# Optimization experiments

Measured on AMD Instinct MI355X. Metric: run time of the kernel, lower is better.

Reference implementation:

```python
import jax, jax.numpy as jnp
import numpy as np

K_TOP = 2          # hardcoded k in MyAttentionFunction
S = 32             # hardcoded spatial size (interpolate to 32x32)
N = S * S          # 1024 patches (patch_size=1, stride=1 unfold)
NEG = jnp.float32(-1e30)  # stand-in for excluding columns from top-k


def setup_inputs() -> dict:
    key = jax.random.key(0)
    k1, k2, k3 = jax.random.split(key, 3)
    C = 4096
    generated = jax.random.normal(k1, (1, C, S, S), dtype=jnp.float32)
    known = jax.random.normal(k2, (1, C, S, S), dtype=jnp.float32)
    mask = jax.random.randint(k3, (1, 1, S, S), 0, 2).astype(jnp.float32)
    return {"generated": generated, "known": known, "mask": mask}


def _forward(generated, known, mask):
    C = generated.shape[1]
    # F.interpolate(mask, (32,32)) nearest, then flatten -> flag in {0,1}, shape (N,)
    flag = jax.image.resize(mask, (1, 1, S, S), method="nearest").reshape(N)
    # MyUnfold(x, 1, 1) == [1, N, C]; drop batch dim of 1.
    P = generated.reshape(C, N).T   # (N, C) patches of `generated`
    Kp = known.reshape(C, N).T      # (N, C) patches of `known`

    norm_p = jnp.sum(P * P, axis=-1)   # (N,)
    norm_k = jnp.sum(Kp * Kp, axis=-1)
    # Full cosine matrices; original restricts rows to flag==1 and columns to
    # flag==0 (cosine0) / flag==1 (cosine1) by extraction; we mask columns with
    # a very negative value so top-k returns the same values with GLOBAL indices
    # (which is exactly what the original reconstructs via nonzero()[indexes]).
    cos0 = (P @ Kp.T) / jnp.sqrt(norm_p[:, None] * norm_k[None, :])  # (N, N)
    cos1 = (P @ P.T) / jnp.sqrt(norm_p[:, None] * norm_p[None, :])
    cos0 = jnp.where(flag[None, :] == 0, cos0, NEG)
    cos1 = jnp.where(flag[None, :] == 1, cos1, NEG)

    w0, i0 = jax.lax.top_k(cos0, K_TOP)  # (N, k) values / global indices
    w1, i1 = jax.lax.top_k(cos1, K_TOP)

    m = flag                      # 1.0 on masked rows
    nm = jnp.sum(m)               # number of masked patches
    # weight means taken only over masked rows, then softmax (original uses
    # .item() + numpy softmax, i.e. detached constants).
    means = jnp.stack(
        [jnp.sum(w0[:, i] * m) / nm for i in range(K_TOP)]
        + [jnp.sum(w1[:, i] * m) / nm for i in range(K_TOP)]
    )
    weights = jax.lax.stop_gradient(jax.nn.softmax(means))  # (2k,)

    # The original builds dense 1024x1024 indicator matrices and bmm's them;
    # each indicator row for a masked patch is one-hot at its retrieved source,
    # so the bmm is just a gather into masked rows. The advanced-indexing quirk
    # ind[mask_idx, src_idx] (nonzero() pairs include a leading 0 column) also
    # unconditionally sets ind[0,0]=1; we reproduce that (set semantics: no
    # double count if row 0 already maps to column 0).
    rtn = jnp.zeros((N, C), dtype=generated.dtype)
    for i in range(2 * K_TOP):
        src = Kp if i < K_TOP else P
        cols = (i0 if i < K_TOP else i1)[:, i % K_TOP]  # (N,) global indices
        out_i = jnp.where(m[:, None] == 1, src[cols], 0.0)  # masked rows only
        dup = 1.0 - ((m[0] == 1) & (cols[0] == 0)).astype(src.dtype)
        out_i = out_i.at[0].add(src[0] * dup)  # spurious ind[0,0]=1 artifact
        rtn = rtn + weights[i] * out_i

    rtn = rtn.reshape(1, S, S, C).transpose(0, 3, 1, 2)  # (1, C, 32, 32)
    return jnp.concatenate([generated, known, rtn], axis=1)


def reference(generated, known, mask):
    return _forward(generated, known, mask)
```

## Files before the change

### kernel.cpp

```cpp
#include <hip/hip_runtime.h>
#include <hip/hip_bf16.h>
#include <math.h>

#define N_TOT 1024
#define C_DIM 4096
#define T_MARGIN 3e-4f

typedef __attribute__((ext_vector_type(8))) _Float16 half8;
typedef __attribute__((ext_vector_type(8))) unsigned short ushort8;
typedef __attribute__((ext_vector_type(4))) float floatx4;

__device__ inline unsigned short f2h(float v) {
    _Float16 h = (_Float16)v;
    return __builtin_bit_cast(unsigned short, h);
}
__device__ inline float h2f(unsigned short u) {
    return (float)__builtin_bit_cast(_Float16, u);
}

__global__ __launch_bounds__(256) void split_norms(const float* __restrict__ G,
                                                   const float* __restrict__ Kn,
                                                   unsigned short* __restrict__ Phi,
                                                   unsigned short* __restrict__ Plo,
                                                   unsigned short* __restrict__ Khi,
                                                   unsigned short* __restrict__ Klo,
                                                   float* __restrict__ normP,
                                                   float* __restrict__ normK) {
    const int z = blockIdx.z;
    const float* X = z ? Kn : G;
    unsigned short* Xhi = z ? Khi : Phi;
    unsigned short* Xlo = z ? Klo : Plo;
    float* normX = z ? normK : normP;

    __shared__ float tile[64 * 65];
    __shared__ float np[256];
    const int t  = threadIdx.x;
    const int c0 = blockIdx.x * 64;
    const int n0 = blockIdx.y * 64;

    float s2 = 0.0f;
    #pragma unroll
    for (int s = 0; s < 16; s++) {
        int c_loc = s * 4 + (t >> 6);
        int n_loc = t & 63;
        float v = X[(c0 + c_loc) * N_TOT + n0 + n_loc];
        tile[c_loc * 65 + n_loc] = v;
        s2 = fmaf(v, v, s2);
    }
    np[t] = s2;
    __syncthreads();

    if (t < 64) {
        float tot = np[t] + np[t + 64] + np[t + 128] + np[t + 192];
        atomicAdd(&normX[n0 + t], tot);
    }

    #pragma unroll
    for (int s = 0; s < 4; s++) {
        int n_loc = s * 16 + (t >> 4);
        int c4    = (t & 15) * 4;
        unsigned short h[4], l[4];
        #pragma unroll
        for (int e = 0; e < 4; e++) {
            float v = tile[(c4 + e) * 65 + n_loc];
            h[e] = f2h(v);
            l[e] = f2h(v - h2f(h[e]));
        }
        size_t base = (size_t)(n0 + n_loc) * C_DIM + c0 + c4;
        *(ushort4*)&Xhi[base] = make_ushort4(h[0], h[1], h[2], h[3]);
        *(ushort4*)&Xlo[base] = make_ushort4(l[0], l[1], l[2], l[3]);
    }
}

__global__ __launch_bounds__(256, 2) void gemm_coarse(const unsigned short* __restrict__ Phi,
                                                      const unsigned short* __restrict__ Bcat,
                                                      float* __restrict__ dotAll) {
    __shared__ unsigned short sA[128 * 64];
    __shared__ unsigned short sB[128 * 64];

    const int t    = threadIdx.x;
    const int wave = t >> 6, lane = t & 63;
    const int wm   = wave >> 1, wn = wave & 1;
    const int quad = lane >> 4, lrow = lane & 15;
    const int ib = blockIdx.x * 128, jb = blockIdx.y * 128;
    const int k_beg = blockIdx.z * 1024;

    const int srow = t >> 3;
    const int g    = (t & 7) ^ (srow & 7);

    const unsigned short* gA = Phi  + (size_t)(ib + srow) * C_DIM + g * 8;
    const unsigned short* gB = Bcat + (size_t)(jb + srow) * C_DIM + g * 8;
    const size_t rstep = (size_t)32 * C_DIM;

    floatx4 acc[4][4] = {};

    for (int k0 = k_beg; k0 < k_beg + 1024; k0 += 64) {
        #pragma unroll
        for (int q = 0; q < 4; q++) {
            int lds_off = q * 4096 + t * 16;
            __builtin_amdgcn_global_load_lds(
                (const __attribute__((address_space(1))) void*)(gA + q * rstep + k0),
                (__attribute__((address_space(3))) void*)((char*)sA + lds_off), 16, 0, 0);
            __builtin_amdgcn_global_load_lds(
                (const __attribute__((address_space(1))) void*)(gB + q * rstep + k0),
                (__attribute__((address_space(3))) void*)((char*)sB + lds_off), 16, 0, 0);
        }
        __syncthreads();

        #pragma unroll
        for (int kk = 0; kk < 2; kk++) {
            const int gk = kk * 4 + quad;
            half8 a[4], b[4];
            #pragma unroll
            for (int ti = 0; ti < 4; ti++) {
                int m = wm * 64 + ti * 16 + lrow;
                a[ti] = *(const half8*)&sA[m * 64 + ((gk ^ (m & 7)) << 3)];
            }
            #pragma unroll
            for (int tj = 0; tj < 4; tj++) {
                int n = wn * 64 + tj * 16 + lrow;
                b[tj] = *(const half8*)&sB[n * 64 + ((gk ^ (n & 7)) << 3)];
            }
            #pragma unroll
            for (int ti = 0; ti < 4; ti++)
                #pragma unroll
                for (int tj = 0; tj < 4; tj++)
                    acc[ti][tj] = __builtin_amdgcn_mfma_f32_16x16x32_f16(a[ti], b[tj], acc[ti][tj], 0, 0, 0);
        }
        __syncthreads();
    }

    #pragma unroll
    for (int tj = 0; tj < 4; tj++) {
        int j = jb + wn * 64 + tj * 16 + lrow;
        #pragma unroll
        for (int ti = 0; ti < 4; ti++) {
            #pragma unroll
            for (int reg = 0; reg < 4; reg++) {
                int i = ib + wm * 64 + ti * 16 + quad * 4 + reg;
                atomicAdd(&dotAll[(size_t)i * 2048 + j], acc[ti][tj][reg]);
            }
        }
    }
}

__global__ __launch_bounds__(256) void topk_refine(const float* __restrict__ dotAll,
                                                   const unsigned short* __restrict__ Phi,
                                                   const unsigned short* __restrict__ Plo,
                                                   const unsigned short* __restrict__ Khi,
                                                   const unsigned short* __restrict__ Klo,
                                                   const float* __restrict__ normP,
                                                   const float* __restrict__ normK,
                                                   const float* __restrict__ flag,
                                                   float* __restrict__ w01,
                                                   int* __restrict__ i01) {
    __shared__ float sAf[C_DIM];
    __shared__ float s_bv[4];
    __shared__ int   s_bj[4];
    __shared__ float s_rcv[8];

    const int row = blockIdx.x;
    const int z   = blockIdx.y;
    const int t   = threadIdx.x;
    const int wave = t >> 6, lane = t & 63;
    const float* D  = dotAll + (size_t)row * 2048 + z * 1024;
    const float* nB = z ? normP : normK;
    const float target = z ? 1.0f : 0.0f;
    const float nr = normP[row];

    float4 dv = *(const float4*)(D + 4 * t);
    float4 fv = *(const float4*)(flag + 4 * t);
    float4 nv = *(const float4*)(nB + 4 * t);
    float cv[4];
    cv[0] = (fv.x == target) ? dv.x * rsqrtf(nr * nv.x) : -INFINITY;
    cv[1] = (fv.y == target) ? dv.y * rsqrtf(nr * nv.y) : -INFINITY;
    cv[2] = (fv.z == target) ? dv.z * rsqrtf(nr * nv.z) : -INFINITY;
    cv[3] = (fv.w == target) ? dv.w * rsqrtf(nr * nv.w) : -INFINITY;

    int   cand[8];
    float cval[8];
    #pragma unroll
    for (int it = 0; it < 8; it++) {
        float bv = cv[0]; int bj = 4 * t;
        #pragma unroll
        for (int e = 1; e < 4; e++) {
            int j = 4 * t + e;
            if (cv[e] > bv || (cv[e] == bv && j < bj)) { bv = cv[e]; bj = j; }
        }
        #pragma unroll
        for (int off = 32; off > 0; off >>= 1) {
            float ov = __shfl_xor(bv, off);
            int   oj = __shfl_xor(bj, off);
            if (ov > bv || (ov == bv && oj < bj)) { bv = ov; bj = oj; }
        }
        if (lane == 0) { s_bv[wave] = bv; s_bj[wave] = bj; }
        __syncthreads();
        float wv = s_bv[0]; int wj = s_bj[0];
        #pragma unroll
        for (int w = 1; w < 4; w++) {
            if (s_bv[w] > wv || (s_bv[w] == wv && s_bj[w] < wj)) { wv = s_bv[w]; wj = s_bj[w]; }
        }
        cand[it] = wj; cval[it] = wv;
        #pragma unroll
        for (int e = 0; e < 4; e++)
            if (wj == 4 * t + e) cv[e] = -INFINITY;
        __syncthreads();
    }

    const bool trust = (cval[0] - cval[1] > T_MARGIN) && (cval[1] - cval[2] > T_MARGIN);
    if (trust) {
        if (t == 0) {
            int base = (z * N_TOT + row) * 2;
            w01[base]     = cval[0];
            w01[base + 1] = cval[1];
            i01[base]     = cand[0];
            i01[base + 1] = cand[1];
        }
        return;
    }

    const unsigned short* Ah = Phi + (size_t)row * C_DIM;
    const unsigned short* Al = Plo + (size_t)row * C_DIM;
    const unsigned short* Bh = z ? Phi : Khi;
    const unsigned short* Bl = z ? Plo : Klo;

    #pragma unroll
    for (int s = 0; s < 2; s++) {
        int c = t * 16 + s * 8;
        ushort8 hb = *(const ushort8*)&Ah[c];
        ushort8 lb = *(const ushort8*)&Al[c];
        #pragma unroll
        for (int e = 0; e < 8; e++) sAf[c + e] = h2f(hb[e]) + h2f(lb[e]);
    }
    __syncthreads();

    const int grp = t >> 5, l32 = t & 31;
    const unsigned short* bh_row = Bh + (size_t)cand[grp] * C_DIM;
    const unsigned short* bl_row = Bl + (size_t)cand[grp] * C_DIM;
    float acc = 0.0f;
    for (int it = 0; it < 16; it++) {
        int c = it * 256 + l32 * 8;
        ushort8 hb = *(const ushort8*)&bh_row[c];
        ushort8 lb = *(const ushort8*)&bl_row[c];
        #pragma unroll
        for (int e = 0; e < 8; e++)
            acc = fmaf(sAf[c + e], h2f(hb[e]) + h2f(lb[e]), acc);
    }
    #pragma unroll
    for (int off = 16; off > 0; off >>= 1) acc += __shfl_xor(acc, off);
    if (l32 == 0) s_rcv[grp] = acc;
    __syncthreads();

    if (t == 0) {
        float v1 = -INFINITY, v2 = -INFINITY;
        int   j1 = 0x7FFFFFFF, j2 = 0x7FFFFFFF;
        #pragma unroll
        for (int q = 0; q < 8; q++) {
            int j = cand[q];
            float cvx = s_rcv[q] * rsqrtf(nr * nB[j]);
            if (cvx > v1 || (cvx == v1 && j < j1)) {
                v2 = v1; j2 = j1; v1 = cvx; j1 = j;
            } else if (cvx > v2 || (cvx == v2 && j < j2)) {
                v2 = cvx; j2 = j;
            }
        }
        int base = (z * N_TOT + row) * 2;
        w01[base]     = v1;
        w01[base + 1] = v2;
        i01[base]     = j1;
        i01[base + 1] = j2;
    }
}

__global__ __launch_bounds__(256) void output_kernel(const float* __restrict__ G,
                                                     const float* __restrict__ Kn,
                                                     const float* __restrict__ flag,
                                                     const float* __restrict__ w01,
                                                     const int* __restrict__ i01,
                                                     float* __restrict__ out) {
    __shared__ float red[5][4];
    __shared__ float wts[4];
    const int c  = blockIdx.x;
    const int t  = threadIdx.x;
    const int n4 = t * 4;

    float4 fv = *(const float4*)&flag[n4];
    const float fa[4] = {fv.x, fv.y, fv.z, fv.w};

    float pm[5] = {};
    #pragma unroll
    for (int e = 0; e < 4; e++) {
        int n = n4 + e;
        float m = fa[e];
        pm[0] += m;
        pm[1] += m * w01[n * 2 + 0];
        pm[2] += m * w01[n * 2 + 1];
        pm[3] += m * w01[2 * N_TOT + n * 2 + 0];
        pm[4] += m * w01[2 * N_TOT + n * 2 + 1];
    }
    #pragma unroll
    for (int i = 0; i < 5; i++)
        #pragma unroll
        for (int off = 32; off > 0; off >>= 1)
            pm[i] += __shfl_xor(pm[i], off);
    const int wave = t >> 6, lane = t & 63;
    if (lane == 0) {
        #pragma unroll
        for (int i = 0; i < 5; i++) red[i][wave] = pm[i];
    }
    __syncthreads();
    if (t == 0) {
        float tot[5];
        #pragma unroll
        for (int i = 0; i < 5; i++)
            tot[i] = red[i][0] + red[i][1] + red[i][2] + red[i][3];
        float inv = 1.0f / tot[0];
        float mv[4] = {tot[1] * inv, tot[2] * inv, tot[3] * inv, tot[4] * inv};
        float mx = fmaxf(fmaxf(mv[0], mv[1]), fmaxf(mv[2], mv[3]));
        float e[4], s = 0.0f;
        #pragma unroll
        for (int q = 0; q < 4; q++) { e[q] = expf(mv[q] - mx); s += e[q]; }
        #pragma unroll
        for (int q = 0; q < 4; q++) wts[q] = e[q] / s;
    }
    __syncthreads();
    const float w0 = wts[0], w1 = wts[1], w2 = wts[2], w3 = wts[3];

    float4 gv = *(const float4*)&G[c * N_TOT + n4];
    float4 kv = *(const float4*)&Kn[c * N_TOT + n4];
    *(float4*)&out[c * N_TOT + n4] = gv;
    *(float4*)&out[C_DIM * N_TOT + c * N_TOT + n4] = kv;

    float val[4];
    #pragma unroll
    for (int e = 0; e < 4; e++) {
        int n = n4 + e;
        float v = 0.0f;
        if (fa[e] == 1.0f) {
            int c00 = i01[n * 2 + 0];
            int c01 = i01[n * 2 + 1];
            int c10 = i01[2 * N_TOT + n * 2 + 0];
            int c11 = i01[2 * N_TOT + n * 2 + 1];
            v = w0 * Kn[c * N_TOT + c00] + w1 * Kn[c * N_TOT + c01]
              + w2 * G[c * N_TOT + c10]  + w3 * G[c * N_TOT + c11];
        }
        if (n == 0) {
            bool m0 = (flag[0] == 1.0f);
            int c00 = i01[0], c01 = i01[1];
            int c10 = i01[2 * N_TOT], c11 = i01[2 * N_TOT + 1];
            float kn0 = Kn[c * N_TOT];
            float g0  = G[c * N_TOT];
            if (!(m0 && c00 == 0)) v += w0 * kn0;
            if (!(m0 && c01 == 0)) v += w1 * kn0;
            if (!(m0 && c10 == 0)) v += w2 * g0;
            if (!(m0 && c11 == 0)) v += w3 * g0;
        }
        val[e] = v;
    }
    *(float4*)&out[2 * C_DIM * N_TOT + c * N_TOT + n4] =
        make_float4(val[0], val[1], val[2], val[3]);
}

extern "C" void kernel_launch(void* const* d_in, const int* in_sizes, int n_in,
                              void* d_out, int out_size, void* d_ws, size_t ws_size,
                              hipStream_t stream) {
    const float* G    = (const float*)d_in[0];
    const float* Kn   = (const float*)d_in[1];
    const float* flag = (const float*)d_in[2];
    float* out = (float*)d_out;

    unsigned short* Khi = (unsigned short*)d_ws;
    unsigned short* Phi = Khi + (size_t)N_TOT * C_DIM;
    unsigned short* Klo = Phi + (size_t)N_TOT * C_DIM;
    unsigned short* Plo = Klo + (size_t)N_TOT * C_DIM;
    float* dotAll = (float*)(Plo + (size_t)N_TOT * C_DIM);
    float* normP  = dotAll + (size_t)N_TOT * 2048;
    float* normK  = normP + N_TOT;
    float* w01    = normK + N_TOT;
    int*   i01    = (int*)(w01 + 4 * N_TOT);

    const size_t zero_bytes = ((size_t)N_TOT * 2048 + 2 * N_TOT) * sizeof(float);
    hipMemsetAsync(dotAll, 0, zero_bytes, stream);

    split_norms<<<dim3(64, 16, 2), 256, 0, stream>>>(G, Kn, Phi, Plo, Khi, Klo, normP, normK);
    gemm_coarse<<<dim3(8, 16, 4), 256, 0, stream>>>(Phi, Khi , dotAll);
    topk_refine<<<dim3(1024, 2), 256, 0, stream>>>(dotAll, Phi, Plo, Khi, Klo,
                                                   normP, normK, flag, w01, i01);
    output_kernel<<<4096, 256, 0, stream>>>(G, Kn, flag, w01, i01, out);
}
```

Before: 188.0 us.

## Compact columns by flag to halve GEMM work and quantize low residuals to int8

```diff
diff --git a/kernel.cpp b/kernel.cpp
--- a/kernel.cpp
+++ b/kernel.cpp
@@ -8,6 +8,7 @@
 
 typedef __attribute__((ext_vector_type(8))) _Float16 half8;
 typedef __attribute__((ext_vector_type(8))) unsigned short ushort8;
+typedef __attribute__((ext_vector_type(8))) char schar8;
 typedef __attribute__((ext_vector_type(4))) float floatx4;
 
 __device__ inline unsigned short f2h(float v) {
@@ -17,19 +18,60 @@
 __device__ inline float h2f(unsigned short u) {
     return (float)__builtin_bit_cast(_Float16, u);
 }
+__device__ inline char lo_enc(float v, unsigned short h) {
+    int e = (h >> 10) & 31;
+    float lo = v - h2f(h);
+    float q = rintf(lo * 240.0f * __uint_as_float((unsigned)(152 - e) << 23));
+    q = fmaxf(-127.0f, fminf(127.0f, q));
+    return (char)(int)q;
+}
+__device__ inline float lo_dec(char q, unsigned short h) {
+    int e = (h >> 10) & 31;
+    return (float)q * __uint_as_float((unsigned)(e + 102) << 23) * (1.0f / 240.0f);
+}
+
+__global__ __launch_bounds__(256) void flagscan(const float* __restrict__ flag,
+                                                int* __restrict__ colidx,
+                                                int* __restrict__ n0p) {
+    __shared__ int cz[256];
+    __shared__ int co[256];
+    const int t = threadIdx.x;
+    float4 fv = *(const float4*)&flag[4 * t];
+    int f[4] = {fv.x == 0.0f, fv.y == 0.0f, fv.z == 0.0f, fv.w == 0.0f};
+    int nz = f[0] + f[1] + f[2] + f[3];
+    cz[t] = nz; co[t] = 4 - nz;
+    __syncthreads();
+    for (int off = 1; off < 256; off <<= 1) {
+        int vz = (t >= off) ? cz[t - off] : 0;
+        int vo = (t >= off) ? co[t - off] : 0;
+        __syncthreads();
+        cz[t] += vz; co[t] += vo;
+        __syncthreads();
+    }
+    const int n0 = cz[255];
+    int zs = cz[t] - nz;
+    int os = n0 + co[t] - (4 - nz);
+    #pragma unroll
+    for (int e = 0; e < 4; e++) {
+        int j = 4 * t + e;
+        if (f[e]) colidx[zs++] = j;
+        else      colidx[os++] = j;
+    }
+    if (t == 0) *n0p = n0;
+}
 
 __global__ __launch_bounds__(256) void split_norms(const float* __restrict__ G,
                                                    const float* __restrict__ Kn,
                                                    unsigned short* __restrict__ Phi,
-                                                   unsigned short* __restrict__ Plo,
+                                                   char* __restrict__ Plo,
                                                    unsigned short* __restrict__ Khi,
-                                                   unsigned short* __restrict__ Klo,
+                                                   char* __restrict__ Klo,
                                                    float* __restrict__ normP,
                                                    float* __restrict__ normK) {
     const int z = blockIdx.z;
     const float* X = z ? Kn : G;
     unsigned short* Xhi = z ? Khi : Phi;
-    unsigned short* Xlo = z ? Klo : Plo;
+    char* Xlo = z ? Klo : Plo;
     float* normX = z ? normK : normP;
 
     __shared__ float tile[64 * 65];
@@ -59,61 +101,72 @@
     for (int s = 0; s < 4; s++) {
         int n_loc = s * 16 + (t >> 4);
         int c4    = (t & 15) * 4;
-        unsigned short h[4], l[4];
+        unsigned short h[4]; char l[4];
         #pragma unroll
         for (int e = 0; e < 4; e++) {
             float v = tile[(c4 + e) * 65 + n_loc];
             h[e] = f2h(v);
-            l[e] = f2h(v - h2f(h[e]));
+            l[e] = lo_enc(v, h[e]);
         }
         size_t base = (size_t)(n0 + n_loc) * C_DIM + c0 + c4;
         *(ushort4*)&Xhi[base] = make_ushort4(h[0], h[1], h[2], h[3]);
-        *(ushort4*)&Xlo[base] = make_ushort4(l[0], l[1], l[2], l[3]);
-    }
-}
-
-__global__ __launch_bounds__(256, 2) void gemm_coarse(const unsigned short* __restrict__ Phi,
-                                                      const unsigned short* __restrict__ Bcat,
-                                                      float* __restrict__ dotAll) {
-    __shared__ unsigned short sA[128 * 64];
+        *(char4*)&Xlo[base]   = make_char4(l[0], l[1], l[2], l[3]);
+    }
+}
+
+__global__ __launch_bounds__(256, 4) void gemm_coarse(const unsigned short* __restrict__ Phi,
+                                                      const unsigned short* __restrict__ Khi,
+                                                      const int* __restrict__ colidx,
+                                                      const int* __restrict__ n0p,
+                                                      float* __restrict__ dotSel) {
+    __shared__ unsigned short sA[64 * 64];
     __shared__ unsigned short sB[128 * 64];
 
     const int t    = threadIdx.x;
     const int wave = t >> 6, lane = t & 63;
     const int wm   = wave >> 1, wn = wave & 1;
     const int quad = lane >> 4, lrow = lane & 15;
-    const int ib = blockIdx.x * 128, jb = blockIdx.y * 128;
-    const int k_beg = blockIdx.z * 1024;
+    const int ib = blockIdx.x * 64, jb = blockIdx.y * 128;
+    const int k_beg = blockIdx.z * 512;
+    const int n0 = *n0p;
 
     const int srow = t >> 3;
     const int g    = (t & 7) ^ (srow & 7);
 
-    const unsigned short* gA = Phi  + (size_t)(ib + srow) * C_DIM + g * 8;
-    const unsigned short* gB = Bcat + (size_t)(jb + srow) * C_DIM + g * 8;
-    const size_t rstep = (size_t)32 * C_DIM;
-
-    floatx4 acc[4][4] = {};
-
-    for (int k0 = k_beg; k0 < k_beg + 1024; k0 += 64) {
-        #pragma unroll
-        for (int q = 0; q < 4; q++) {
-            int lds_off = q * 4096 + t * 16;
+    const unsigned short* gA[2];
+    gA[0] = Phi + (size_t)(ib + srow) * C_DIM + g * 8;
+    gA[1] = gA[0] + (size_t)32 * C_DIM;
+    const unsigned short* gB[4];
+    #pragma unroll
+    for (int q = 0; q < 4; q++) {
+        int s = jb + q * 32 + srow;
+        int row = colidx[s];
+        const unsigned short* src = (s < n0) ? Khi : Phi;
+        gB[q] = src + (size_t)row * C_DIM + g * 8;
+    }
+
+    floatx4 acc[2][4] = {};
+
+    for (int k0 = k_beg; k0 < k_beg + 512; k0 += 64) {
+        #pragma unroll
+        for (int q = 0; q < 2; q++)
             __builtin_amdgcn_global_load_lds(
-                (const __attribute__((address_space(1))) void*)(gA + q * rstep + k0),
-                (__attribute__((address_space(3))) void*)((char*)sA + lds_off), 16, 0, 0);
+                (const __attribute__((address_space(1))) void*)(gA[q] + k0),
+                (__attribute__((address_space(3))) void*)((char*)sA + q * 4096 + t * 16), 16, 0, 0);
+        #pragma unroll
+        for (int q = 0; q < 4; q++)
             __builtin_amdgcn_global_load_lds(
-                (const __attribute__((address_space(1))) void*)(gB + q * rstep + k0),
-                (__attribute__((address_space(3))) void*)((char*)sB + lds_off), 16, 0, 0);
-        }
+                (const __attribute__((address_space(1))) void*)(gB[q] + k0),
+                (__attribute__((address_space(3))) void*)((char*)sB + q * 4096 + t * 16), 16, 0, 0);
         __syncthreads();
 
         #pragma unroll
         for (int kk = 0; kk < 2; kk++) {
             const int gk = kk * 4 + quad;
-            half8 a[4], b[4];
+            half8 a[2], b[4];
             #pragma unroll
-            for (int ti = 0; ti < 4; ti++) {
-                int m = wm * 64 + ti * 16 + lrow;
+            for (int ti = 0; ti < 2; ti++) {
+                int m = wm * 32 + ti * 16 + lrow;
                 a[ti] = *(const half8*)&sA[m * 64 + ((gk ^ (m & 7)) << 3)];
             }
             #pragma unroll
@@ -122,7 +175,7 @@
                 b[tj] = *(const half8*)&sB[n * 64 + ((gk ^ (n & 7)) << 3)];
             }
             #pragma unroll
-            for (int ti = 0; ti < 4; ti++)
+            for (int ti = 0; ti < 2; ti++)
                 #pragma unroll
                 for (int tj = 0; tj < 4; tj++)
                     acc[ti][tj] = __builtin_amdgcn_mfma_f32_16x16x32_f16(a[ti], b[tj], acc[ti][tj], 0, 0, 0);
@@ -134,24 +187,25 @@
     for (int tj = 0; tj < 4; tj++) {
         int j = jb + wn * 64 + tj * 16 + lrow;
         #pragma unroll
-        for (int ti = 0; ti < 4; ti++) {
+        for (int ti = 0; ti < 2; ti++) {
             #pragma unroll
             for (int reg = 0; reg < 4; reg++) {
-                int i = ib + wm * 64 + ti * 16 + quad * 4 + reg;
-                atomicAdd(&dotAll[(size_t)i * 2048 + j], acc[ti][tj][reg]);
+                int i = ib + wm * 32 + ti * 16 + quad * 4 + reg;
+                atomicAdd(&dotSel[(size_t)i * N_TOT + j], acc[ti][tj][reg]);
             }
         }
     }
 }
 
-__global__ __launch_bounds__(256) void topk_refine(const float* __restrict__ dotAll,
+__global__ __launch_bounds__(256) void topk_refine(const float* __restrict__ dotSel,
                                                    const unsigned short* __restrict__ Phi,
-                                                   const unsigned short* __restrict__ Plo,
+                                                   const char* __restrict__ Plo,
                                                    const unsigned short* __restrict__ Khi,
-                                                   const unsigned short* __restrict__ Klo,
+                                                   const char* __restrict__ Klo,
                                                    const float* __restrict__ normP,
                                                    const float* __restrict__ normK,
-                                                   const float* __restrict__ flag,
+                                                   const int* __restrict__ colidx,
+                                                   const int* __restrict__ n0p,
                                                    float* __restrict__ w01,
                                                    int* __restrict__ i01) {
     __shared__ float sAf[C_DIM];
@@ -163,19 +217,21 @@
     const int z   = blockIdx.y;
     const int t   = threadIdx.x;
     const int wave = t >> 6, lane = t & 63;
-    const float* D  = dotAll + (size_t)row * 2048 + z * 1024;
-    const float* nB = z ? normP : normK;
-    const float target = z ? 1.0f : 0.0f;
+    const int n0 = *n0p;
     const float nr = normP[row];
 
-    float4 dv = *(const float4*)(D + 4 * t);
-    float4 fv = *(const float4*)(flag + 4 * t);
-    float4 nv = *(const float4*)(nB + 4 * t);
+    float4 dv = *(const float4*)&dotSel[(size_t)row * N_TOT + 4 * t];
     float cv[4];
-    cv[0] = (fv.x == target) ? dv.x * rsqrtf(nr * nv.x) : -INFINITY;
-    cv[1] = (fv.y == target) ? dv.y * rsqrtf(nr * nv.y) : -INFINITY;
-    cv[2] = (fv.z == target) ? dv.z * rsqrtf(nr * nv.z) : -INFINITY;
-    cv[3] = (fv.w == target) ? dv.w * rsqrtf(nr * nv.w) : -INFINITY;
+    #pragma unroll
+    for (int e = 0; e < 4; e++) {
+        int s = 4 * t + e;
+        bool inz = z ? (s >= n0) : (s < n0);
+        if (inz) {
+            int gj = colidx[s];
+            float nb = (s < n0) ? normK[gj] : normP[gj];
+            cv[e] = dv[e] * rsqrtf(nr * nb);
+        } else cv[e] = -INFINITY;
+    }
 
     int   cand[8];
     float cval[8];
@@ -197,9 +253,8 @@
         __syncthreads();
         float wv = s_bv[0]; int wj = s_bj[0];
         #pragma unroll
-        for (int w = 1; w < 4; w++) {
+        for (int w = 1; w < 4; w++)
             if (s_bv[w] > wv || (s_bv[w] == wv && s_bj[w] < wj)) { wv = s_bv[w]; wj = s_bj[w]; }
-        }
         cand[it] = wj; cval[it] = wv;
         #pragma unroll
         for (int e = 0; e < 4; e++)
@@ -213,38 +268,39 @@
             int base = (z * N_TOT + row) * 2;
             w01[base]     = cval[0];
             w01[base + 1] = cval[1];
-            i01[base]     = cand[0];
-            i01[base + 1] = cand[1];
+            i01[base]     = colidx[cand[0]];
+            i01[base + 1] = colidx[cand[1]];
         }
         return;
     }
 
-    const unsigned short* Ah = Phi + (size_t)row * C_DIM;
-    const unsigned short* Al = Plo + (size_t)row * C_DIM;
-    const unsigned short* Bh = z ? Phi : Khi;
-    const unsigned short* Bl = z ? Plo : Klo;
-
-    #pragma unroll
-    for (int s = 0; s < 2; s++) {
-        int c = t * 16 + s * 8;
-        ushort8 hb = *(const ushort8*)&Ah[c];
-        ushort8 lb = *(const ushort8*)&Al[c];
-        #pragma unroll
-        for (int e = 0; e < 8; e++) sAf[c + e] = h2f(hb[e]) + h2f(lb[e]);
+    {
+        const unsigned short* Ah = Phi + (size_t)row * C_DIM;
+        const char*           Al = Plo + (size_t)row * C_DIM;
+        #pragma unroll
+        for (int s = 0; s < 2; s++) {
+            int c = t * 16 + s * 8;
+            ushort8 hb = *(const ushort8*)&Ah[c];
+            schar8  lb = *(const schar8*)&Al[c];
+            #pragma unroll
+            for (int e = 0; e < 8; e++) sAf[c + e] = h2f(hb[e]) + lo_dec(lb[e], hb[e]);
+        }
     }
     __syncthreads();
 
     const int grp = t >> 5, l32 = t & 31;
-    const unsigned short* bh_row = Bh + (size_t)cand[grp] * C_DIM;
-    const unsigned short* bl_row = Bl + (size_t)cand[grp] * C_DIM;
+    const int cs  = cand[grp];
+    const int gj  = colidx[cs];
+    const unsigned short* bh_row = ((cs < n0) ? Khi : Phi) + (size_t)gj * C_DIM;
+    const char*           bl_row = ((cs < n0) ? Klo : Plo) + (size_t)gj * C_DIM;
     float acc = 0.0f;
     for (int it = 0; it < 16; it++) {
         int c = it * 256 + l32 * 8;
         ushort8 hb = *(const ushort8*)&bh_row[c];
-        ushort8 lb = *(const ushort8*)&bl_row[c];
+        schar8  lb = *(const schar8*)&bl_row[c];
         #pragma unroll
         for (int e = 0; e < 8; e++)
-            acc = fmaf(sAf[c + e], h2f(hb[e]) + h2f(lb[e]), acc);
+            acc = fmaf(sAf[c + e], h2f(hb[e]) + lo_dec(lb[e], hb[e]), acc);
     }
     #pragma unroll
     for (int off = 16; off > 0; off >>= 1) acc += __shfl_xor(acc, off);
@@ -256,8 +312,12 @@
         int   j1 = 0x7FFFFFFF, j2 = 0x7FFFFFFF;
         #pragma unroll
         for (int q = 0; q < 8; q++) {
-            int j = cand[q];
-            float cvx = s_rcv[q] * rsqrtf(nr * nB[j]);
+            if (!(cval[q] > -1e29f)) continue;
+            int s = cand[q];
+            int gjx = colidx[s];
+            float nb = (s < n0) ? normK[gjx] : normP[gjx];
+            float cvx = s_rcv[q] * rsqrtf(nr * nb);
+            int j = gjx;
             if (cvx > v1 || (cvx == v1 && j < j1)) {
                 v2 = v1; j2 = j1; v1 = cvx; j1 = j;
             } else if (cvx > v2 || (cvx == v2 && j < j2)) {
@@ -369,22 +429,26 @@
     const float* flag = (const float*)d_in[2];
     float* out = (float*)d_out;
 
-    unsigned short* Khi = (unsigned short*)d_ws;
-    unsigned short* Phi = Khi + (size_t)N_TOT * C_DIM;
-    unsigned short* Klo = Phi + (size_t)N_TOT * C_DIM;
-    unsigned short* Plo = Klo + (size_t)N_TOT * C_DIM;
-    float* dotAll = (float*)(Plo + (size_t)N_TOT * C_DIM);
-    float* normP  = dotAll + (size_t)N_TOT * 2048;
-    float* normK  = normP + N_TOT;
-    float* w01    = normK + N_TOT;
-    int*   i01    = (int*)(w01 + 4 * N_TOT);
-
-    const size_t zero_bytes = ((size_t)N_TOT * 2048 + 2 * N_TOT) * sizeof(float);
-    hipMemsetAsync(dotAll, 0, zero_bytes, stream);
-
+    char* p = (char*)d_ws;
+    unsigned short* Phi = (unsigned short*)p;  p += (size_t)N_TOT * C_DIM * 2;
+    unsigned short* Khi = (unsigned short*)p;  p += (size_t)N_TOT * C_DIM * 2;
+    char* Plo = p;                             p += (size_t)N_TOT * C_DIM;
+    char* Klo = p;                             p += (size_t)N_TOT * C_DIM;
+    float* dotSel = (float*)p;                 p += (size_t)N_TOT * N_TOT * 4;
+    float* normP  = (float*)p;                 p += N_TOT * 4;
+    float* normK  = (float*)p;                 p += N_TOT * 4;
+    float* w01    = (float*)p;                 p += 4 * N_TOT * 4;
+    int*   i01    = (int*)p;                   p += 4 * N_TOT * 4;
+    int*   colidx = (int*)p;                   p += N_TOT * 4;
+    int*   n0p    = (int*)p;
+
+    const size_t zero_bytes = ((size_t)N_TOT * N_TOT + 2 * N_TOT) * sizeof(float);
+    hipMemsetAsync(dotSel, 0, zero_bytes, stream);
+
+    flagscan<<<1, 256, 0, stream>>>(flag, colidx, n0p);
     split_norms<<<dim3(64, 16, 2), 256, 0, stream>>>(G, Kn, Phi, Plo, Khi, Klo, normP, normK);
-    gemm_coarse<<<dim3(8, 16, 4), 256, 0, stream>>>(Phi, Khi , dotAll);
-    topk_refine<<<dim3(1024, 2), 256, 0, stream>>>(dotAll, Phi, Plo, Khi, Klo,
-                                                   normP, normK, flag, w01, i01);
+    gemm_coarse<<<dim3(16, 8, 8), 256, 0, stream>>>(Phi, Khi, colidx, n0p, dotSel);
+    topk_refine<<<dim3(1024, 2), 256, 0, stream>>>(dotSel, Phi, Plo, Khi, Klo,
+                                                   normP, normK, colidx, n0p, w01, i01);
     output_kernel<<<4096, 256, 0, stream>>>(G, Kn, flag, w01, i01, out);
 }
```

New measurement: 186.0 us. No clear change (-1.1%).
